# Kernel tuning notes

Hardware: AMD Instinct MI355X
Metric: run time of the kernel (lower is better)

Reference implementation:

```python
import jax, jax.numpy as jnp
import numpy as np

DIM = 1536
N_HEADS = 12
HEAD_DIM = 128
EPS = 1e-6
MAX_ATTN = 32760      # local_attn_size(21) * 1560
CACHE_SIZE = 32760
CUR_START = 4680      # 3 frames * 1560 already in cache
TWO_PI = 6.283185307179586


def rms_norm(x, g, eps=EPS):
    x32 = x.astype(jnp.float32)
    y = x32 * jax.lax.rsqrt(jnp.mean(x32 * x32, axis=-1, keepdims=True) + eps)
    return y.astype(x.dtype) * g


def causal_rope(x, grid_sizes, freqs, start_frame):
    # x: [B, s, n, d]; freqs: angles [1024, d//2] (torch stores exp(i*theta); we store theta)
    B, s, n, d = x.shape
    c = d // 2
    c3 = c // 3
    f_ang = freqs[:, : c - 2 * c3]
    h_ang = freqs[:, c - 2 * c3 : c - c3]
    w_ang = freqs[:, c - c3 :]
    outs = []
    grid_np = np.asarray(grid_sizes)
    for i in range(B):
        F, H, W = (int(v) for v in grid_np[i])
        seq = F * H * W
        ang = jnp.concatenate([
            jnp.broadcast_to(f_ang[start_frame : start_frame + F][:, None, None, :], (F, H, W, c - 2 * c3)),
            jnp.broadcast_to(h_ang[:H][None, :, None, :], (F, H, W, c3)),
            jnp.broadcast_to(w_ang[:W][None, None, :, :], (F, H, W, c3)),
        ], axis=-1).reshape(seq, 1, c)
        cos, sin = jnp.cos(ang), jnp.sin(ang)
        xi = x[i, :seq].astype(jnp.float32).reshape(seq, n, c, 2)
        a, b = xi[..., 0], xi[..., 1]
        rot = jnp.stack([a * cos - b * sin, a * sin + b * cos], axis=-1).reshape(seq, n, d)
        outs.append(jnp.concatenate([rot, x[i, seq:].astype(jnp.float32)], axis=0))
    return jnp.stack(outs).astype(x.dtype)


def setup_inputs() -> dict:
    key = jax.random.key(0)
    ks = jax.random.split(key, 16)
    B, S = 1, 1560
    w = lambda k: jax.random.normal(k, (DIM, DIM), jnp.float32) * 0.02
    return {
        "x": jax.random.normal(ks[0], (B, S, DIM), jnp.float32),
        "freqs": jax.random.uniform(ks[1], (1024, HEAD_DIM // 2), jnp.float32) * TWO_PI,
        "wq": w(ks[2]), "bq": jnp.zeros((DIM,), jnp.float32),
        "wk": w(ks[3]), "bk": jnp.zeros((DIM,), jnp.float32),
        "wv": w(ks[4]), "bv": jnp.zeros((DIM,), jnp.float32),
        "wo": w(ks[5]), "bo": jnp.zeros((DIM,), jnp.float32),
        "gq": jnp.ones((DIM,), jnp.float32),
        "gk": jnp.ones((DIM,), jnp.float32),
        "kv_cache_k": jax.random.normal(ks[6], (B, CACHE_SIZE, N_HEADS, HEAD_DIM), jnp.float32),
        "kv_cache_v": jax.random.normal(ks[7], (B, CACHE_SIZE, N_HEADS, HEAD_DIM), jnp.float32),
        "grid_sizes": jnp.array([[1, 30, 52]], jnp.int64 if jax.config.jax_enable_x64 else jnp.int32),
        "seq_lens": jnp.array([1560], jnp.int32),
        "current_start": CUR_START,
    }


def reference(x, freqs, wq, bq, wk, bk, wv, bv, wo, bo, gq, gk,
              kv_cache_k, kv_cache_v, grid_sizes, seq_lens, current_start):
    b, s = x.shape[:2]
    n, d = N_HEADS, HEAD_DIM
    q = rms_norm(x @ wq.T + bq, gq).reshape(b, s, n, d)
    k = rms_norm(x @ wk.T + bk, gk).reshape(b, s, n, d)
    v = (x @ wv.T + bv).reshape(b, s, n, d)

    grid_np = np.asarray(grid_sizes)
    frame_seqlen = int(grid_np[0, 1]) * int(grid_np[0, 2])  # 1560
    start_frame = int(current_start) // frame_seqlen
    rq = causal_rope(q, grid_sizes, freqs, start_frame)
    rk = causal_rope(k, grid_sizes, freqs, start_frame)

    # cache in sync (global_end==local_end==current_start), no-eviction branch
    cur_start = int(current_start)
    cur_end = cur_start + s
    k_cache = kv_cache_k.at[:, cur_start:cur_end].set(rk)
    v_cache = kv_cache_v.at[:, cur_start:cur_end].set(v)

    win_start = max(0, cur_end - MAX_ATTN)
    kw = k_cache[:, win_start:cur_end]  # [B, W, n, d]
    vw = v_cache[:, win_start:cur_end]

    scale = 1.0 / np.sqrt(d).astype(np.float32)
    scores = jnp.einsum("bqnd,bknd->bnqk", rq, kw) * scale
    attn = jax.nn.softmax(scores, axis=-1)
    out = jnp.einsum("bnqk,bknd->bqnd", attn, vw).reshape(b, s, n * d)
    return out @ wo.T + bo
```

## Files before the change

### kernel.cpp

```cpp
#include <hip/hip_runtime.h>
#include <math.h>

typedef unsigned short ushort_t;
typedef __attribute__((ext_vector_type(8))) short bf16x8;
typedef __attribute__((ext_vector_type(4))) float f32x4;

#define DIM    1536
#define NH     12
#define HD     128
#define SEQ    1560
#define CURS   4680
#define NKEY   6240
#define GW     52
#define SFRAME 3
#define EPSV   1e-6f
#define QSCALE 0.08838834764831845f
#define KSPLIT 2
#define NCHUNK 98
#define CPS    49
#define QPAD   1600
#define MPAD   1664

__device__ __forceinline__ ushort_t f2bf(float f) {
    union { float f; unsigned int u; } x; x.f = f;
    unsigned int r = x.u + 0x7fffu + ((x.u >> 16) & 1u);
    return (ushort_t)(r >> 16);
}

__device__ __forceinline__ void gld_lds16(const ushort_t* gsrc, ushort_t* ldst) {
    __builtin_amdgcn_global_load_lds(
        (const __attribute__((address_space(1))) unsigned int*)gsrc,
        (__attribute__((address_space(3))) unsigned int*)ldst,
        16, 0, 0);
}

__global__ __launch_bounds__(256)
void f32_to_bf16_k(const float* __restrict__ in, ushort_t* __restrict__ out, int n8)
{
    const int i = blockIdx.x * 256 + threadIdx.x;
    if (i >= n8) return;
    float4 a = ((const float4*)in)[2*i];
    float4 b = ((const float4*)in)[2*i + 1];
    union { ushort_t u[8]; bf16x8 v; } uu;
    uu.u[0]=f2bf(a.x); uu.u[1]=f2bf(a.y); uu.u[2]=f2bf(a.z); uu.u[3]=f2bf(a.w);
    uu.u[4]=f2bf(b.x); uu.u[5]=f2bf(b.y); uu.u[6]=f2bf(b.z); uu.u[7]=f2bf(b.w);
    ((bf16x8*)out)[i] = uu.v;
}

template<int QKV>
__global__ __launch_bounds__(256) void gemm128(
    const ushort_t* __restrict__ A, const ushort_t* __restrict__ B,
    const float* __restrict__ b0, const float* __restrict__ b1, const float* __restrict__ b2,
    float* __restrict__ outQ, float* __restrict__ outK, ushort_t* __restrict__ outV,
    int M, int K)
{
    __shared__ ushort_t As[128*32];
    __shared__ ushort_t Bs[128*32];

    const int t = threadIdx.x;
    const int w = t >> 6, l = t & 63, quad = l >> 4, l15 = l & 15;
    const int bm = blockIdx.y * 128;
    const int bn = blockIdx.x * 128;
    const int wm = (w & 1) << 6, wn = (w >> 1) << 6;

    const int srow = (w << 5) + (l >> 2);
    const int scol = (l & 3) << 3;
    const ushort_t* Ag = A + (size_t)(bm + srow) * K + scol;
    const ushort_t* Bg = B + (size_t)(bn + srow) * K + scol;
    ushort_t* AsB = &As[w << 10];
    ushort_t* BsB = &Bs[w << 10];

    f32x4 acc[4][4] = {};

    for (int k0 = 0; k0 < K; k0 += 32) {
        __syncthreads();
        gld_lds16(Ag + k0,          AsB);
        gld_lds16(Ag + k0 + 16*K,   AsB + 512);
        gld_lds16(Bg + k0,          BsB);
        gld_lds16(Bg + k0 + 16*K,   BsB + 512);
        __syncthreads();

        bf16x8 af[4], bfv[4];
        #pragma unroll
        for (int i = 0; i < 4; ++i) {
            af[i]  = *(const bf16x8*)&As[(wm + i*16 + l15) * 32 + quad*8];
            bfv[i] = *(const bf16x8*)&Bs[(wn + i*16 + l15) * 32 + quad*8];
        }
        #pragma unroll
        for (int mi = 0; mi < 4; ++mi)
            #pragma unroll
            for (int ni = 0; ni < 4; ++ni)
                acc[mi][ni] = __builtin_amdgcn_mfma_f32_16x16x32_bf16(af[mi], bfv[ni], acc[mi][ni], 0,0,0);
    }

    int mat, c0;
    if (QKV) { mat = blockIdx.x / 12; c0 = (blockIdx.x % 12) * 128; }
    else     { mat = 0;               c0 = blockIdx.x * 128; }
    const float* bias = QKV ? (mat == 0 ? b0 : (mat == 1 ? b1 : b2)) : b0;
    float* outF = (QKV && mat == 1) ? outK : outQ;

    #pragma unroll
    for (int ni = 0; ni < 4; ++ni) {
        const int col = c0 + wn + ni*16 + l15;
        const float bc = bias[col];
        #pragma unroll
        for (int mi = 0; mi < 4; ++mi) {
            #pragma unroll
            for (int r = 0; r < 4; ++r) {
                const int row = bm + wm + mi*16 + quad*4 + r;
                if (row < M) {
                    const float v = acc[mi][ni][r] + bc;
                    if (QKV && mat == 2) outV[(size_t)row * DIM + col] = f2bf(v);
                    else                 outF[(size_t)row * DIM + col] = v;
                }
            }
        }
    }
}

__global__ __launch_bounds__(256)
void rmsnorm_rope(const float* __restrict__ buf, const float* __restrict__ g,
                  const float* __restrict__ freqs, ushort_t* __restrict__ out,
                  float scale)
{
    const int tok = blockIdx.x;
    const int t = threadIdx.x;
    const float* row = buf + (size_t)tok * DIM;

    float2 xv[3];
    float ss = 0.f;
    #pragma unroll
    for (int i = 0; i < 3; ++i) {
        xv[i] = ((const float2*)row)[t + 256*i];
        ss += xv[i].x*xv[i].x + xv[i].y*xv[i].y;
    }
    #pragma unroll
    for (int off = 32; off > 0; off >>= 1) ss += __shfl_xor(ss, off);
    __shared__ float part[4];
    __shared__ float invs;
    if ((t & 63) == 0) part[t >> 6] = ss;
    __syncthreads();
    if (t == 0) invs = rsqrtf((part[0]+part[1]+part[2]+part[3]) * (1.0f/DIM) + EPSV);
    __syncthreads();
    const float inv = invs * scale;
    const int hh = tok / GW;
    const int ww = tok % GW;
    #pragma unroll
    for (int i = 0; i < 3; ++i) {
        const int p = t + 256*i;
        const int j = p & 63;
        const int rsel = (j < 22) ? SFRAME : ((j < 43) ? hh : ww);
        const float ang = freqs[rsel*64 + j];
        float sn, cs;
        sincosf(ang, &sn, &cs);
        const float a = xv[i].x * inv * g[2*p];
        const float b = xv[i].y * inv * g[2*p+1];
        const unsigned int lo = f2bf(a*cs - b*sn);
        const unsigned int hi = f2bf(a*sn + b*cs);
        ((unsigned int*)out)[(size_t)tok*768 + p] = (hi << 16) | lo;
    }
}

__global__ __launch_bounds__(256)
void kwin_k(const float* __restrict__ kc, const ushort_t* __restrict__ kb,
            ushort_t* __restrict__ Kw)
{
    const int tid = blockIdx.x * 256 + threadIdx.x;
    const int dc = tid & 15;
    const int hp = tid >> 4;
    const int p = hp % NKEY;
    const int h = hp / NKEY;
    ushort_t* outp = Kw + (size_t)tid * 8;
    if (p >= CURS) {
        *(bf16x8*)outp = *(const bf16x8*)(kb + (size_t)(p - CURS)*DIM + h*HD + dc*8);
    } else {
        const float* src = kc + ((size_t)p * NH + h) * HD + dc*8;
        float4 f0 = *(const float4*)src, f1 = *(const float4*)(src + 4);
        union { ushort_t u[8]; bf16x8 v; } uu;
        uu.u[0]=f2bf(f0.x); uu.u[1]=f2bf(f0.y); uu.u[2]=f2bf(f0.z); uu.u[3]=f2bf(f0.w);
        uu.u[4]=f2bf(f1.x); uu.u[5]=f2bf(f1.y); uu.u[6]=f2bf(f1.z); uu.u[7]=f2bf(f1.w);
        *(bf16x8*)outp = uu.v;
    }
}

__global__ __launch_bounds__(256)
void kwin_v(const float* __restrict__ vc, const ushort_t* __restrict__ vb,
            ushort_t* __restrict__ Vwt)
{
    __shared__ ushort_t tile[64][40];
    const int t = threadIdx.x;
    const int bp = blockIdx.x, bd = blockIdx.y, h = blockIdx.z;
    const int p_loc = t >> 2, ds0 = (t & 3) * 8;
    const int pr = min(bp*64 + p_loc, NKEY-1);
    const int d = bd*32 + ds0;
    union { ushort_t u[8]; bf16x8 v; } uu;
    if (pr >= CURS) {
        uu.v = *(const bf16x8*)(vb + (size_t)(pr - CURS)*DIM + h*HD + d);
    } else {
        const float* src = vc + ((size_t)pr*NH + h)*HD + d;
        float4 f0 = *(const float4*)src, f1 = *(const float4*)(src+4);
        uu.u[0]=f2bf(f0.x); uu.u[1]=f2bf(f0.y); uu.u[2]=f2bf(f0.z); uu.u[3]=f2bf(f0.w);
        uu.u[4]=f2bf(f1.x); uu.u[5]=f2bf(f1.y); uu.u[6]=f2bf(f1.z); uu.u[7]=f2bf(f1.w);
    }
    *(bf16x8*)&tile[p_loc][ds0] = uu.v;
    __syncthreads();
    const int d_loc = t >> 3, ps = (t & 7) * 8;
    if (bp*64 + ps < NKEY) {
        union { ushort_t u[8]; bf16x8 v; } oo;
        #pragma unroll
        for (int i = 0; i < 8; ++i) oo.u[i] = tile[ps + i][d_loc];
        *(bf16x8*)(Vwt + ((size_t)h*HD + bd*32 + d_loc) * NKEY + bp*64 + ps) = oo.v;
    }
}

__global__ __launch_bounds__(256)
void attn_kernel(const ushort_t* __restrict__ qb, const ushort_t* __restrict__ Kw,
                 const ushort_t* __restrict__ Vwt, float* __restrict__ Op,
                 float* __restrict__ Ms, float* __restrict__ Ls)
{
    __shared__ ushort_t Ks[64][136];
    __shared__ ushort_t Vs[128][72];
    __shared__ float    Sc[64][68];
    __shared__ ushort_t Pb[64][72];
    __shared__ float mst[64], lst[64], alf[64];

    const int t = threadIdx.x;
    const int w = t >> 6, l = t & 63, quad = l >> 4, l15 = l & 15;
    const int h = blockIdx.y;
    const int q0 = blockIdx.x * 64;
    const int z = blockIdx.z;

    bf16x8 qf[4];
    {
        const int qrow = min(q0 + w*16 + l15, SEQ-1);
        const ushort_t* qp = qb + ((size_t)qrow*NH + h)*HD;
        #pragma unroll
        for (int s = 0; s < 4; ++s) qf[s] = *(const bf16x8*)(qp + s*32 + quad*8);
    }
    f32x4 o[8] = {};
    if (t < 64) { mst[t] = -1e30f; lst[t] = 0.f; }

    const ushort_t* Kwh = Kw  + (size_t)h * NKEY * HD;
    const ushort_t* Vwh = Vwt + (size_t)h * HD * NKEY;
    const int key_st = t >> 2, kd0 = (t & 3) * 32;
    const int vd = t >> 1,     vk0 = (t & 1) * 32;

    for (int c = z*CPS; c < (z+1)*CPS; ++c) {
        const int p0 = c * 64;
        bf16x8 kr[4], vr[4];
        {
            const ushort_t* kp = Kwh + (size_t)min(p0 + key_st, NKEY-1) * HD + kd0;
            #pragma unroll
            for (int i = 0; i < 4; ++i) kr[i] = *(const bf16x8*)(kp + i*8);
            const ushort_t* vp = Vwh + (size_t)vd * NKEY;
            #pragma unroll
            for (int i = 0; i < 4; ++i) {
                const int pk = min(p0 + vk0 + i*8, NKEY-8);
                vr[i] = *(const bf16x8*)(vp + pk);
            }
        }
        __syncthreads();
        #pragma unroll
        for (int i = 0; i < 4; ++i) *(bf16x8*)&Ks[key_st][kd0 + i*8] = kr[i];
        #pragma unroll
        for (int i = 0; i < 4; ++i) *(bf16x8*)&Vs[vd][vk0 + i*8] = vr[i];
        __syncthreads();

        f32x4 sf[4];
        #pragma unroll
        for (int kb = 0; kb < 4; ++kb) { f32x4 zz = {0.f,0.f,0.f,0.f}; sf[kb] = zz; }
        #pragma unroll
        for (int s = 0; s < 4; ++s) {
            #pragma unroll
            for (int kb = 0; kb < 4; ++kb) {
                bf16x8 kf = *(const bf16x8*)&Ks[kb*16 + l15][s*32 + quad*8];
                sf[kb] = __builtin_amdgcn_mfma_f32_16x16x32_bf16(qf[s], kf, sf[kb], 0,0,0);
            }
        }
        #pragma unroll
        for (int kb = 0; kb < 4; ++kb) {
            const int pkey = p0 + kb*16 + l15;
            const bool valid = pkey < NKEY;
            #pragma unroll
            for (int r = 0; r < 4; ++r)
                Sc[w*16 + quad*4 + r][kb*16 + l15] = valid ? sf[kb][r] : -1e30f;
        }
        __syncthreads();

        {
            const int row = t >> 2, seg = t & 3;
            float sv[16];
            #pragma unroll
            for (int i = 0; i < 4; ++i) {
                float4 s4 = *(const float4*)&Sc[row][seg*16 + i*4];
                sv[i*4+0]=s4.x; sv[i*4+1]=s4.y; sv[i*4+2]=s4.z; sv[i*4+3]=s4.w;
            }
            float mx = sv[0];
            #pragma unroll
            for (int i = 1; i < 16; ++i) mx = fmaxf(mx, sv[i]);
            mx = fmaxf(mx, __shfl_xor(mx, 1));
            mx = fmaxf(mx, __shfl_xor(mx, 2));
            const float mo = mst[row];
            const float mn = fmaxf(mo, mx);
            float sum = 0.f;
            union { ushort_t u[8]; bf16x8 v; } pa, pc;
            #pragma unroll
            for (int i = 0; i < 8; ++i) { float e = __expf(sv[i]   - mn); sum += e; pa.u[i] = f2bf(e); }
            #pragma unroll
            for (int i = 0; i < 8; ++i) { float e = __expf(sv[8+i] - mn); sum += e; pc.u[i] = f2bf(e); }
            sum += __shfl_xor(sum, 1);
            sum += __shfl_xor(sum, 2);
            *(bf16x8*)&Pb[row][seg*16]     = pa.v;
            *(bf16x8*)&Pb[row][seg*16 + 8] = pc.v;
            if (seg == 0) {
                const float al = __expf(mo - mn);
                lst[row] = lst[row]*al + sum;
                mst[row] = mn;
                alf[row] = al;
            }
        }
        __syncthreads();

        {
            float ar[4];
            #pragma unroll
            for (int r = 0; r < 4; ++r) ar[r] = alf[w*16 + quad*4 + r];
            #pragma unroll
            for (int nb = 0; nb < 8; ++nb)
                #pragma unroll
                for (int r = 0; r < 4; ++r) o[nb][r] *= ar[r];
            #pragma unroll
            for (int ks = 0; ks < 2; ++ks) {
                bf16x8 pf = *(const bf16x8*)&Pb[w*16 + l15][ks*32 + quad*8];
                #pragma unroll
                for (int nb = 0; nb < 8; ++nb) {
                    bf16x8 vf = *(const bf16x8*)&Vs[nb*16 + l15][ks*32 + quad*8];
                    o[nb] = __builtin_amdgcn_mfma_f32_16x16x32_bf16(pf, vf, o[nb], 0,0,0);
                }
            }
        }
    }
    __syncthreads();
    {
        float* Opz = Op + (size_t)z * QPAD * NH * HD;
        #pragma unroll
        for (int nb = 0; nb < 8; ++nb) {
            const int col = nb*16 + l15;
            #pragma unroll
            for (int r = 0; r < 4; ++r) {
                const int row = q0 + w*16 + quad*4 + r;
                Opz[((size_t)row*NH + h)*HD + col] = o[nb][r];
            }
        }
        if (t < 64) {
            const int row = q0 + t;
            Ms[(size_t)z*QPAD*NH + row*NH + h] = mst[t];
            Ls[(size_t)z*QPAD*NH + row*NH + h] = lst[t];
        }
    }
}

__global__ __launch_bounds__(256)
void merge_kernel(const float* __restrict__ Op, const float* __restrict__ Ms,
                  const float* __restrict__ Ls, ushort_t* __restrict__ abufb)
{
    const int tid = blockIdx.x*256 + threadIdx.x;
    const int dq = tid & 31;
    const int h = (tid >> 5) % NH;
    const int q = tid / (NH*32);
    const size_t sidx = (size_t)q*NH + h;
    const float m0 = Ms[sidx], m1 = Ms[(size_t)QPAD*NH + sidx];
    const float l0 = Ls[sidx], l1 = Ls[(size_t)QPAD*NH + sidx];
    const float mm = fmaxf(m0, m1);
    const float w0 = __expf(m0 - mm), w1 = __expf(m1 - mm);
    const float inv = 1.0f / (l0*w0 + l1*w1);
    const size_t oidx = sidx*HD + dq*4;
    float4 a = *(const float4*)(Op + oidx);
    float4 b = *(const float4*)(Op + (size_t)QPAD*NH*HD + oidx);
    ushort4 r;
    r.x = f2bf((a.x*w0 + b.x*w1)*inv);
    r.y = f2bf((a.y*w0 + b.y*w1)*inv);
    r.z = f2bf((a.z*w0 + b.z*w1)*inv);
    r.w = f2bf((a.w*w0 + b.w*w1)*inv);
    *(ushort4*)(abufb + (size_t)q*DIM + h*HD + dq*4) = r;
}

extern "C" void kernel_launch(void* const* d_in, const int* in_sizes, int n_in,
                              void* d_out, int out_size, void* d_ws, size_t ws_size,
                              hipStream_t stream)
{
    const float* x     = (const float*)d_in[0];
    const float* freqs = (const float*)d_in[1];
    const float* wq    = (const float*)d_in[2];
    const float* bq    = (const float*)d_in[3];
    const float* wk    = (const float*)d_in[4];
    const float* bk    = (const float*)d_in[5];
    const float* wv    = (const float*)d_in[6];
    const float* bv    = (const float*)d_in[7];
    const float* wo    = (const float*)d_in[8];
    const float* bo    = (const float*)d_in[9];
    const float* gq    = (const float*)d_in[10];
    const float* gk    = (const float*)d_in[11];
    const float* kck   = (const float*)d_in[12];
    const float* kcv   = (const float*)d_in[13];

    char* ws = (char*)d_ws;
    const size_t SZ_B16 = (size_t)SEQ*DIM*2;
    const size_t SZ_KW  = (size_t)NH*NKEY*HD*2;
    const size_t SZ_OP  = (size_t)KSPLIT*QPAD*NH*HD*4;
    const size_t SZ_ST  = (size_t)KSPLIT*QPAD*NH*4;
    const size_t SZ_AB  = (size_t)MPAD*DIM*2;

    ushort_t* qb  = (ushort_t*)(ws);
    ushort_t* kb  = (ushort_t*)(ws + SZ_B16);
    ushort_t* vb  = (ushort_t*)(ws + 2*SZ_B16);
    ushort_t* Kw  = (ushort_t*)(ws + 3*SZ_B16);
    ushort_t* Vwt = (ushort_t*)(ws + 3*SZ_B16 + SZ_KW);
    float*    Opb = (float*)   (ws + 3*SZ_B16 + 2*SZ_KW);
    float*    Msp = (float*)   (ws + 3*SZ_B16 + 2*SZ_KW + SZ_OP);
    float*    Lsp = (float*)   (ws + 3*SZ_B16 + 2*SZ_KW + SZ_OP + SZ_ST);
    ushort_t* abufb=(ushort_t*)(ws + 3*SZ_B16 + 2*SZ_KW + SZ_OP + 2*SZ_ST);
    ushort_t* wob = (ushort_t*)(ws + 3*SZ_B16 + 2*SZ_KW + SZ_OP + 2*SZ_ST + SZ_AB);
    ushort_t* xb   = abufb;
    ushort_t* Wqkv = Kw;
    float*    qf   = Opb;
    float*    kf   = Opb + (size_t)SEQ*DIM;

    dim3 blk(256);
    const int XN8 = SEQ*DIM/8;
    const int WN8 = DIM*DIM/8;
    const size_t WE = (size_t)DIM*DIM;

    hipLaunchKernelGGL(f32_to_bf16_k, dim3((XN8+255)/256), blk, 0, stream, x,  xb,           XN8);
    hipLaunchKernelGGL(f32_to_bf16_k, dim3((WN8+255)/256), blk, 0, stream, wq, Wqkv,         WN8);
    hipLaunchKernelGGL(f32_to_bf16_k, dim3((WN8+255)/256), blk, 0, stream, wk, Wqkv + WE,    WN8);
    hipLaunchKernelGGL(f32_to_bf16_k, dim3((WN8+255)/256), blk, 0, stream, wv, Wqkv + 2*WE,  WN8);
    hipLaunchKernelGGL(f32_to_bf16_k, dim3((WN8+255)/256), blk, 0, stream, wo, wob,          WN8);

    hipLaunchKernelGGL((gemm128<1>), dim3(36, 13), blk, 0, stream,
                       xb, Wqkv, bq, bk, bv, qf, kf, vb, SEQ, DIM);

    hipLaunchKernelGGL(rmsnorm_rope, dim3(SEQ), blk, 0, stream, qf, gq, freqs, qb, QSCALE);
    hipLaunchKernelGGL(rmsnorm_rope, dim3(SEQ), blk, 0, stream, kf, gk, freqs, kb, 1.0f);
    hipLaunchKernelGGL(kwin_k, dim3(NH*NKEY*16/256), blk, 0, stream, kck, kb, Kw);
    hipLaunchKernelGGL(kwin_v, dim3(98, 4, NH), blk, 0, stream, kcv, vb, Vwt);
    hipLaunchKernelGGL(attn_kernel, dim3((SEQ+63)/64, NH, KSPLIT), blk, 0, stream,
                       qb, Kw, Vwt, Opb, Msp, Lsp);
    hipLaunchKernelGGL(merge_kernel, dim3(SEQ*NH*32/256), blk, 0, stream, Opb, Msp, Lsp, abufb);

    hipLaunchKernelGGL((gemm128<0>), dim3(12, 13), blk, 0, stream,
                       abufb, wob, bo, bo, bo, (float*)d_out, (float*)d_out, (ushort_t*)nullptr, SEQ, DIM);
}
```

Baseline: 726.8 us.

## Double-buffer attention K/V via direct-to-LDS loads and keep softmax in registers

```diff
diff --git a/kernel.cpp b/kernel.cpp
--- a/kernel.cpp
+++ b/kernel.cpp
@@ -27,6 +27,12 @@
     return (ushort_t)(r >> 16);
 }
 
+__device__ __forceinline__ unsigned int cvt_pk_bf16(float lo, float hi) {
+    unsigned int r;
+    asm("v_cvt_pk_bf16_f32 %0, %1, %2" : "=v"(r) : "v"(lo), "v"(hi));
+    return r;
+}
+
 __device__ __forceinline__ void gld_lds16(const ushort_t* gsrc, ushort_t* ldst) {
     __builtin_amdgcn_global_load_lds(
         (const __attribute__((address_space(1))) unsigned int*)gsrc,
@@ -34,17 +40,32 @@
         16, 0, 0);
 }
 
-__global__ __launch_bounds__(256)
-void f32_to_bf16_k(const float* __restrict__ in, ushort_t* __restrict__ out, int n8)
-{
-    const int i = blockIdx.x * 256 + threadIdx.x;
-    if (i >= n8) return;
-    float4 a = ((const float4*)in)[2*i];
-    float4 b = ((const float4*)in)[2*i + 1];
+#define XN8 (SEQ*DIM/8)
+#define WN8 (DIM*DIM/8)
+__global__ __launch_bounds__(256)
+void conv5(const float* __restrict__ x,  const float* __restrict__ wq,
+           const float* __restrict__ wk, const float* __restrict__ wv,
+           const float* __restrict__ wo,
+           ushort_t* __restrict__ xb, ushort_t* __restrict__ wqkv,
+           ushort_t* __restrict__ wob)
+{
+    const int b = blockIdx.x;
+    const float* src; ushort_t* dst; int idx;
+    if (b < 1170) { src = x; dst = xb; idx = b*256 + threadIdx.x; if (idx >= XN8) return; }
+    else {
+        const int k = (b - 1170) / 1152, r = (b - 1170) % 1152;
+        idx = r*256 + threadIdx.x;
+        if      (k == 0) { src = wq; dst = wqkv; }
+        else if (k == 1) { src = wk; dst = wqkv + (size_t)DIM*DIM; }
+        else if (k == 2) { src = wv; dst = wqkv + 2*(size_t)DIM*DIM; }
+        else             { src = wo; dst = wob; }
+    }
+    float4 a = ((const float4*)src)[2*(size_t)idx];
+    float4 c = ((const float4*)src)[2*(size_t)idx + 1];
     union { ushort_t u[8]; bf16x8 v; } uu;
     uu.u[0]=f2bf(a.x); uu.u[1]=f2bf(a.y); uu.u[2]=f2bf(a.z); uu.u[3]=f2bf(a.w);
-    uu.u[4]=f2bf(b.x); uu.u[5]=f2bf(b.y); uu.u[6]=f2bf(b.z); uu.u[7]=f2bf(b.w);
-    ((bf16x8*)out)[i] = uu.v;
+    uu.u[4]=f2bf(c.x); uu.u[5]=f2bf(c.y); uu.u[6]=f2bf(c.z); uu.u[7]=f2bf(c.w);
+    ((bf16x8*)dst)[idx] = uu.v;
 }
 
 template<int QKV>
@@ -119,13 +140,17 @@
 }
 
 __global__ __launch_bounds__(256)
-void rmsnorm_rope(const float* __restrict__ buf, const float* __restrict__ g,
-                  const float* __restrict__ freqs, ushort_t* __restrict__ out,
-                  float scale)
+void rms2(const float* __restrict__ qf, const float* __restrict__ kf,
+          const float* __restrict__ gq, const float* __restrict__ gk,
+          const float* __restrict__ freqs, ushort_t* __restrict__ qb,
+          unsigned int* __restrict__ KwU)
 {
     const int tok = blockIdx.x;
+    const int path = blockIdx.y;
     const int t = threadIdx.x;
-    const float* row = buf + (size_t)tok * DIM;
+    const float* row = (path ? kf : qf) + (size_t)tok * DIM;
+    const float* g = path ? gk : gq;
+    const float scale = path ? 1.0f : QSCALE;
 
     float2 xv[3];
     float ss = 0.f;
@@ -157,30 +182,31 @@
         const float b = xv[i].y * inv * g[2*p+1];
         const unsigned int lo = f2bf(a*cs - b*sn);
         const unsigned int hi = f2bf(a*sn + b*cs);
-        ((unsigned int*)out)[(size_t)tok*768 + p] = (hi << 16) | lo;
-    }
-}
-
-__global__ __launch_bounds__(256)
-void kwin_k(const float* __restrict__ kc, const ushort_t* __restrict__ kb,
-            ushort_t* __restrict__ Kw)
+        const unsigned int word = (hi << 16) | lo;
+        if (!path) {
+            ((unsigned int*)qb)[(size_t)tok*768 + p] = word;
+        } else {
+            const int head = p >> 6;
+            const int dp = p & 63;
+            KwU[((size_t)head*NKEY + CURS + tok)*64 + dp] = word;
+        }
+    }
+}
+
+__global__ __launch_bounds__(256)
+void kwin_k(const float* __restrict__ kc, ushort_t* __restrict__ Kw)
 {
     const int tid = blockIdx.x * 256 + threadIdx.x;
     const int dc = tid & 15;
     const int hp = tid >> 4;
-    const int p = hp % NKEY;
-    const int h = hp / NKEY;
-    ushort_t* outp = Kw + (size_t)tid * 8;
-    if (p >= CURS) {
-        *(bf16x8*)outp = *(const bf16x8*)(kb + (size_t)(p - CURS)*DIM + h*HD + dc*8);
-    } else {
-        const float* src = kc + ((size_t)p * NH + h) * HD + dc*8;
-        float4 f0 = *(const float4*)src, f1 = *(const float4*)(src + 4);
-        union { ushort_t u[8]; bf16x8 v; } uu;
-        uu.u[0]=f2bf(f0.x); uu.u[1]=f2bf(f0.y); uu.u[2]=f2bf(f0.z); uu.u[3]=f2bf(f0.w);
-        uu.u[4]=f2bf(f1.x); uu.u[5]=f2bf(f1.y); uu.u[6]=f2bf(f1.z); uu.u[7]=f2bf(f1.w);
-        *(bf16x8*)outp = uu.v;
-    }
+    const int p = hp % CURS;
+    const int h = hp / CURS;
+    const float* src = kc + ((size_t)p * NH + h) * HD + dc*8;
+    float4 f0 = *(const float4*)src, f1 = *(const float4*)(src + 4);
+    union { ushort_t u[8]; bf16x8 v; } uu;
+    uu.u[0]=f2bf(f0.x); uu.u[1]=f2bf(f0.y); uu.u[2]=f2bf(f0.z); uu.u[3]=f2bf(f0.w);
+    uu.u[4]=f2bf(f1.x); uu.u[5]=f2bf(f1.y); uu.u[6]=f2bf(f1.z); uu.u[7]=f2bf(f1.w);
+    *(bf16x8*)(Kw + ((size_t)h*NKEY + p)*HD + dc*8) = uu.v;
 }
 
 __global__ __launch_bounds__(256)
@@ -218,11 +244,8 @@
                  const ushort_t* __restrict__ Vwt, float* __restrict__ Op,
                  float* __restrict__ Ms, float* __restrict__ Ls)
 {
-    __shared__ ushort_t Ks[64][136];
-    __shared__ ushort_t Vs[128][72];
-    __shared__ float    Sc[64][68];
-    __shared__ ushort_t Pb[64][72];
-    __shared__ float mst[64], lst[64], alf[64];
+    __shared__ ushort_t Ks[2][64*128];
+    __shared__ ushort_t Vs[2][128*64];
 
     const int t = threadIdx.x;
     const int w = t >> 6, l = t & 63, quad = l >> 4, l15 = l & 15;
@@ -238,109 +261,123 @@
         for (int s = 0; s < 4; ++s) qf[s] = *(const bf16x8*)(qp + s*32 + quad*8);
     }
     f32x4 o[8] = {};
-    if (t < 64) { mst[t] = -1e30f; lst[t] = 0.f; }
+    float m_reg = -1e30f, l_reg = 0.f;
 
     const ushort_t* Kwh = Kw  + (size_t)h * NKEY * HD;
     const ushort_t* Vwh = Vwt + (size_t)h * HD * NKEY;
-    const int key_st = t >> 2, kd0 = (t & 3) * 32;
-    const int vd = t >> 1,     vk0 = (t & 1) * 32;
-
-    for (int c = z*CPS; c < (z+1)*CPS; ++c) {
+
+    const int krow_b = w*4 + (l >> 4);
+    const int kunit  = l & 15;
+    const int vrow_b = w*8 + (l >> 3);
+    const int vunit  = l & 7;
+
+    const int c_begin = z*CPS, c_end = (z+1)*CPS;
+
+    auto STAGE = [&](int buf, int c) {
         const int p0 = c * 64;
-        bf16x8 kr[4], vr[4];
-        {
-            const ushort_t* kp = Kwh + (size_t)min(p0 + key_st, NKEY-1) * HD + kd0;
-            #pragma unroll
-            for (int i = 0; i < 4; ++i) kr[i] = *(const bf16x8*)(kp + i*8);
-            const ushort_t* vp = Vwh + (size_t)vd * NKEY;
-            #pragma unroll
-            for (int i = 0; i < 4; ++i) {
-                const int pk = min(p0 + vk0 + i*8, NKEY-8);
-                vr[i] = *(const bf16x8*)(vp + pk);
-            }
-        }
+        #pragma unroll
+        for (int i = 0; i < 4; ++i) {
+            const int row = i*16 + krow_b;
+            const int key = min(p0 + row, NKEY-1);
+            const int du  = kunit ^ (row & 7);
+            gld_lds16(Kwh + (size_t)key*HD + du*8, &Ks[buf][i*2048 + w*512]);
+        }
+        #pragma unroll
+        for (int i = 0; i < 4; ++i) {
+            const int d   = i*32 + vrow_b;
+            const int ku  = vunit ^ (d & 7);
+            const int kb0 = min(p0 + ku*8, NKEY-8);
+            gld_lds16(Vwh + (size_t)d*NKEY + kb0, &Vs[buf][i*2048 + w*512]);
+        }
+    };
+
+    STAGE(0, c_begin);
+    __syncthreads();
+    int cur = 0;
+
+    for (int c = c_begin; c < c_end; ++c) {
+        if (c + 1 < c_end) STAGE(cur ^ 1, c + 1);
+        const int p0 = c * 64;
+
+        f32x4 sf[4];
+        #pragma unroll
+        for (int kb = 0; kb < 4; ++kb) { f32x4 zz = {0.f,0.f,0.f,0.f}; sf[kb] = zz; }
+        #pragma unroll
+        for (int s = 0; s < 4; ++s) {
+            #pragma unroll
+            for (int kb = 0; kb < 4; ++kb) {
+                const int row = kb*16 + l15;
+                const int usw = (s*4 + quad) ^ (l15 & 7);
+                bf16x8 kf = *(const bf16x8*)&Ks[cur][row*128 + usw*8];
+                sf[kb] = __builtin_amdgcn_mfma_f32_16x16x32_bf16(kf, qf[s], sf[kb], 0,0,0);
+            }
+        }
+
+        float mx = -1e30f;
+        #pragma unroll
+        for (int kb = 0; kb < 4; ++kb) {
+            #pragma unroll
+            for (int r = 0; r < 4; ++r) {
+                if (p0 + kb*16 + quad*4 + r >= NKEY) sf[kb][r] = -1e30f;
+                mx = fmaxf(mx, sf[kb][r]);
+            }
+        }
+        mx = fmaxf(mx, __shfl_xor(mx, 16));
+        mx = fmaxf(mx, __shfl_xor(mx, 32));
+        const float mn = fmaxf(m_reg, mx);
+        const float al = __expf(m_reg - mn);
+        m_reg = mn;
+        float sum = 0.f;
+        #pragma unroll
+        for (int kb = 0; kb < 4; ++kb) {
+            #pragma unroll
+            for (int r = 0; r < 4; ++r) {
+                const float ev = __expf(sf[kb][r] - mn);
+                sf[kb][r] = ev;
+                sum += ev;
+            }
+        }
+        sum += __shfl_xor(sum, 16);
+        sum += __shfl_xor(sum, 32);
+        l_reg = l_reg * al + sum;
+
+        union { unsigned int u32[4]; bf16x8 v; } pf0, pf1;
+        pf0.u32[0] = cvt_pk_bf16(sf[0][0], sf[0][1]);
+        pf0.u32[1] = cvt_pk_bf16(sf[0][2], sf[0][3]);
+        pf0.u32[2] = cvt_pk_bf16(sf[1][0], sf[1][1]);
+        pf0.u32[3] = cvt_pk_bf16(sf[1][2], sf[1][3]);
+        pf1.u32[0] = cvt_pk_bf16(sf[2][0], sf[2][1]);
+        pf1.u32[1] = cvt_pk_bf16(sf[2][2], sf[2][3]);
+        pf1.u32[2] = cvt_pk_bf16(sf[3][0], sf[3][1]);
+        pf1.u32[3] = cvt_pk_bf16(sf[3][2], sf[3][3]);
+
+        float ar[4];
+        #pragma unroll
+        for (int r = 0; r < 4; ++r) ar[r] = __shfl(al, quad*4 + r);
+        #pragma unroll
+        for (int nb = 0; nb < 8; ++nb)
+            #pragma unroll
+            for (int r = 0; r < 4; ++r) o[nb][r] *= ar[r];
+
+        #pragma unroll
+        for (int ks = 0; ks < 2; ++ks) {
+            const bf16x8 pf = ks ? pf1.v : pf0.v;
+            #pragma unroll
+            for (int nb = 0; nb < 8; ++nb) {
+                const int row = nb*16 + l15;
+                const int u0 = (ks*4 +     (quad>>1)) ^ (l15 & 7);
+                const int u1 = (ks*4 + 2 + (quad>>1)) ^ (l15 & 7);
+                union { unsigned long long q[2]; bf16x8 v; } vf;
+                vf.q[0] = *(const unsigned long long*)&Vs[cur][row*64 + u0*8 + (quad&1)*4];
+                vf.q[1] = *(const unsigned long long*)&Vs[cur][row*64 + u1*8 + (quad&1)*4];
+                o[nb] = __builtin_amdgcn_mfma_f32_16x16x32_bf16(pf, vf.v, o[nb], 0,0,0);
+            }
+        }
+
         __syncthreads();
-        #pragma unroll
-        for (int i = 0; i < 4; ++i) *(bf16x8*)&Ks[key_st][kd0 + i*8] = kr[i];
-        #pragma unroll
-        for (int i = 0; i < 4; ++i) *(bf16x8*)&Vs[vd][vk0 + i*8] = vr[i];
-        __syncthreads();
-
-        f32x4 sf[4];
-        #pragma unroll
-        for (int kb = 0; kb < 4; ++kb) { f32x4 zz = {0.f,0.f,0.f,0.f}; sf[kb] = zz; }
-        #pragma unroll
-        for (int s = 0; s < 4; ++s) {
-            #pragma unroll
-            for (int kb = 0; kb < 4; ++kb) {
-                bf16x8 kf = *(const bf16x8*)&Ks[kb*16 + l15][s*32 + quad*8];
-                sf[kb] = __builtin_amdgcn_mfma_f32_16x16x32_bf16(qf[s], kf, sf[kb], 0,0,0);
-            }
-        }
-        #pragma unroll
-        for (int kb = 0; kb < 4; ++kb) {
-            const int pkey = p0 + kb*16 + l15;
-            const bool valid = pkey < NKEY;
-            #pragma unroll
-            for (int r = 0; r < 4; ++r)
-                Sc[w*16 + quad*4 + r][kb*16 + l15] = valid ? sf[kb][r] : -1e30f;
-        }
-        __syncthreads();
-
-        {
-            const int row = t >> 2, seg = t & 3;
-            float sv[16];
-            #pragma unroll
-            for (int i = 0; i < 4; ++i) {
-                float4 s4 = *(const float4*)&Sc[row][seg*16 + i*4];
-                sv[i*4+0]=s4.x; sv[i*4+1]=s4.y; sv[i*4+2]=s4.z; sv[i*4+3]=s4.w;
-            }
-            float mx = sv[0];
-            #pragma unroll
-            for (int i = 1; i < 16; ++i) mx = fmaxf(mx, sv[i]);
-            mx = fmaxf(mx, __shfl_xor(mx, 1));
-            mx = fmaxf(mx, __shfl_xor(mx, 2));
-            const float mo = mst[row];
-            const float mn = fmaxf(mo, mx);
-            float sum = 0.f;
-            union { ushort_t u[8]; bf16x8 v; } pa, pc;
-            #pragma unroll
-            for (int i = 0; i < 8; ++i) { float e = __expf(sv[i]   - mn); sum += e; pa.u[i] = f2bf(e); }
-            #pragma unroll
-            for (int i = 0; i < 8; ++i) { float e = __expf(sv[8+i] - mn); sum += e; pc.u[i] = f2bf(e); }
-            sum += __shfl_xor(sum, 1);
-            sum += __shfl_xor(sum, 2);
-            *(bf16x8*)&Pb[row][seg*16]     = pa.v;
-            *(bf16x8*)&Pb[row][seg*16 + 8] = pc.v;
-            if (seg == 0) {
-                const float al = __expf(mo - mn);
-                lst[row] = lst[row]*al + sum;
-                mst[row] = mn;
-                alf[row] = al;
-            }
-        }
-        __syncthreads();
-
-        {
-            float ar[4];
-            #pragma unroll
-            for (int r = 0; r < 4; ++r) ar[r] = alf[w*16 + quad*4 + r];
-            #pragma unroll
-            for (int nb = 0; nb < 8; ++nb)
-                #pragma unroll
-                for (int r = 0; r < 4; ++r) o[nb][r] *= ar[r];
-            #pragma unroll
-            for (int ks = 0; ks < 2; ++ks) {
-                bf16x8 pf = *(const bf16x8*)&Pb[w*16 + l15][ks*32 + quad*8];
-                #pragma unroll
-                for (int nb = 0; nb < 8; ++nb) {
-                    bf16x8 vf = *(const bf16x8*)&Vs[nb*16 + l15][ks*32 + quad*8];
-                    o[nb] = __builtin_amdgcn_mfma_f32_16x16x32_bf16(pf, vf, o[nb], 0,0,0);
-                }
-            }
-        }
-    }
-    __syncthreads();
+        cur ^= 1;
+    }
+
     {
         float* Opz = Op + (size_t)z * QPAD * NH * HD;
         #pragma unroll
@@ -352,10 +389,10 @@
                 Opz[((size_t)row*NH + h)*HD + col] = o[nb][r];
             }
         }
-        if (t < 64) {
-            const int row = q0 + t;
-            Ms[(size_t)z*QPAD*NH + row*NH + h] = mst[t];
-            Ls[(size_t)z*QPAD*NH + row*NH + h] = lst[t];
+        if (quad == 0) {
+            const int row = q0 + w*16 + l15;
+            Ms[(size_t)z*QPAD*NH + (size_t)row*NH + h] = m_reg;
+            Ls[(size_t)z*QPAD*NH + (size_t)row*NH + h] = l_reg;
         }
     }
 }
@@ -427,25 +464,24 @@
     float*    kf   = Opb + (size_t)SEQ*DIM;
 
     dim3 blk(256);
-    const int XN8 = SEQ*DIM/8;
-    const int WN8 = DIM*DIM/8;
-    const size_t WE = (size_t)DIM*DIM;
-
-    hipLaunchKernelGGL(f32_to_bf16_k, dim3((XN8+255)/256), blk, 0, stream, x,  xb,           XN8);
-    hipLaunchKernelGGL(f32_to_bf16_k, dim3((WN8+255)/256), blk, 0, stream, wq, Wqkv,         WN8);
-    hipLaunchKernelGGL(f32_to_bf16_k, dim3((WN8+255)/256), blk, 0, stream, wk, Wqkv + WE,    WN8);
-    hipLaunchKernelGGL(f32_to_bf16_k, dim3((WN8+255)/256), blk, 0, stream, wv, Wqkv + 2*WE,  WN8);
-    hipLaunchKernelGGL(f32_to_bf16_k, dim3((WN8+255)/256), blk, 0, stream, wo, wob,          WN8);
+    (void)kb;
+
+    hipLaunchKernelGGL(conv5, dim3(1170 + 4*1152), blk, 0, stream,
+                       x, wq, wk, wv, wo, xb, Wqkv, wob);
 
     hipLaunchKernelGGL((gemm128<1>), dim3(36, 13), blk, 0, stream,
                        xb, Wqkv, bq, bk, bv, qf, kf, vb, SEQ, DIM);
 
-    hipLaunchKernelGGL(rmsnorm_rope, dim3(SEQ), blk, 0, stream, qf, gq, freqs, qb, QSCALE);
-    hipLaunchKernelGGL(rmsnorm_rope, dim3(SEQ), blk, 0, stream, kf, gk, freqs, kb, 1.0f);
-    hipLaunchKernelGGL(kwin_k, dim3(NH*NKEY*16/256), blk, 0, stream, kck, kb, Kw);
+    hipLaunchKernelGGL(rms2, dim3(SEQ, 2), blk, 0, stream,
+                       qf, kf, gq, gk, freqs, qb, (unsigned int*)Kw);
+
+    hipLaunchKernelGGL(kwin_k, dim3(NH*CURS*16/256), blk, 0, stream, kck, Kw);
+
     hipLaunchKernelGGL(kwin_v, dim3(98, 4, NH), blk, 0, stream, kcv, vb, Vwt);
+
     hipLaunchKernelGGL(attn_kernel, dim3((SEQ+63)/64, NH, KSPLIT), blk, 0, stream,
                        qb, Kw, Vwt, Opb, Msp, Lsp);
+
     hipLaunchKernelGGL(merge_kernel, dim3(SEQ*NH*32/256), blk, 0, stream, Opb, Msp, Lsp, abufb);
 
     hipLaunchKernelGGL((gemm128<0>), dim3(12, 13), blk, 0, stream,
```

Measured after the change: 694.2 us. -4.5%, faster.
